# Kernel tuning notes

Hardware: AMD Instinct MI355X
Metric: run time of the kernel (lower is better)

Reference implementation:

```python
import jax, jax.numpy as jnp
import numpy as np

B, S, E, H = 4, 2048, 512, 8
D = E // H  # head dim = 64
# Faithful to torch precedence bug: embed_dim // num_heads ** 0.5 == E // (H**0.5)
SCALE = float(E // H ** 0.5)  # 181.0
EPS = 1e-5


def _ln(x, g, b):
    mu = jnp.mean(x, axis=-1, keepdims=True)
    var = jnp.var(x, axis=-1, keepdims=True)
    return (x - mu) / jnp.sqrt(var + EPS) * g + b


def setup_inputs() -> dict:
    key = jax.random.key(0)
    ks = jax.random.split(key, 14)
    inv = 1.0 / np.sqrt(E)
    inp = {
        'q': jax.random.normal(ks[0], (B, S, E), jnp.float32),
        'k': jax.random.normal(ks[1], (B, S, E), jnp.float32),
        'v': jax.random.normal(ks[2], (B, S, E), jnp.float32),
        'Wq': jax.random.uniform(ks[3], (E, E), jnp.float32, -inv, inv),
        'bq': jnp.zeros((E,), jnp.float32),
        'Wk': jax.random.uniform(ks[4], (E, E), jnp.float32, -inv, inv),
        'bk': jnp.zeros((E,), jnp.float32),
        'Wv': jax.random.uniform(ks[5], (E, E), jnp.float32, -inv, inv),
        'bv': jnp.zeros((E,), jnp.float32),
        'Wo': jax.random.uniform(ks[6], (E, E), jnp.float32, -inv, inv),
        'bo': jnp.zeros((E,), jnp.float32),
        'gq': jnp.ones((D,), jnp.float32), 'betaq': jnp.zeros((D,), jnp.float32),
        'gk': jnp.ones((D,), jnp.float32), 'betak': jnp.zeros((D,), jnp.float32),
        'gv': jnp.ones((D,), jnp.float32), 'betav': jnp.zeros((D,), jnp.float32),
        'query_mask': jax.random.uniform(ks[7], (B, S, 1)) < 0.9,
        'key_mask': jax.random.uniform(ks[8], (B, S, 1)) < 0.9,
        'value_mask': jax.random.uniform(ks[9], (B, S, 1)) < 0.9,
    }
    return inp


def reference(q, k, v, Wq, bq, Wk, bk, Wv, bv, Wo, bo,
              gq, betaq, gk, betak, gv, betav,
              query_mask, key_mask, value_mask):
    # project + mask (bool mask multiplies as 0/1)
    qp = (q @ Wq.T + bq) * query_mask            # [B,S,E]
    kp = (k @ Wk.T + bk) * key_mask
    vp = (v @ Wv.T + bv) * value_mask
    # split heads -> [B,H,S,D]
    split = lambda x: x.reshape(B, -1, H, D).transpose(0, 2, 1, 3)
    qh, kh, vh = split(qp), split(kp), split(vp)
    # middle_norm: per-head LayerNorm over head dim
    qh, kh, vh = _ln(qh, gq, betaq), _ln(kh, gk, betak), _ln(vh, gv, betav)
    scores = jnp.einsum('bhqd,bhkd->bhqk', qh, kh) / SCALE  # [B,H,S,S]
    km = key_mask[:, :, 0][:, None, None, :]     # [B,1,1,S]
    scores = jnp.where(km, scores, -1e9)
    attn = jax.nn.softmax(scores, axis=-1)
    qm = query_mask[:, :, 0][:, None, :, None]   # [B,1,S,1]
    attn = attn * qm                              # zero-fill post-softmax
    out = jnp.einsum('bhqk,bhkd->bhqd', attn, vh)
    out = out.transpose(0, 2, 1, 3).reshape(B, -1, E)
    out = (out @ Wo.T + bo) * query_mask
    return out
```

## Files before the change

### kernel.cpp

```cpp
#include <hip/hip_runtime.h>
#include <cstdint>
#include <cstddef>

#define BB 4
#define SS 2048
#define EE 512
#define HH 8
#define DD 64
#define MM (BB*SS)
#define BHSD ((size_t)BB*HH*SS*DD)

static constexpr float SCALE_INV = 1.0f / 181.0f;
static constexpr float LN_EPS = 1e-5f;

typedef float  v4f  __attribute__((ext_vector_type(4)));
typedef __bf16 v8bf __attribute__((ext_vector_type(8)));
typedef __bf16 v4bf __attribute__((ext_vector_type(4)));
typedef short  s4   __attribute__((ext_vector_type(4)));

static __device__ __forceinline__ v4f mfma16(v8bf a, v8bf b, v4f c) {
  return __builtin_amdgcn_mfma_f32_16x16x32_bf16(a, b, c, 0, 0, 0);
}
static __device__ __forceinline__ v4f mfma16x16(v4bf a, v4bf b, v4f c) {
  s4 ai = __builtin_bit_cast(s4, a);
  s4 bi = __builtin_bit_cast(s4, b);
  return __builtin_amdgcn_mfma_f32_16x16x16bf16_1k(ai, bi, c, 0, 0, 0);
}

typedef const void __attribute__((address_space(1))) gas_void;
typedef void __attribute__((address_space(3))) las_void;
static __device__ __forceinline__ void gload_lds16(const void* g, void* l) {
  __builtin_amdgcn_global_load_lds((gas_void*)g, (las_void*)l, 16, 0, 0);
}

static constexpr size_t oXb = 0;
static constexpr size_t oWb = oXb + (size_t)3*MM*EE*2;
static constexpr size_t oXh = oWb + (size_t)4*EE*EE*2;
static constexpr size_t oAO = oXh + (size_t)3*MM*EE*2;
static constexpr size_t oMk = oAO + (size_t)MM*EE*2;

__global__ void mask_kernel(const void* qm, const void* km, const void* vm, float* maskF) {
  __shared__ int s_n01, s_nF;
  const int t = threadIdx.x;
  if (t == 0) { s_n01 = 0; s_nF = 0; }
  __syncthreads();
  int n01 = 0, nF = 0;
  const unsigned* wq = (const unsigned*)qm;
  for (int i = t; i < 2048; i += 256) {
    const unsigned u = wq[i];
    if (u != 0u && u != 1u) n01 = 1;
    if (u != 0u && u != 0x3F800000u) nF = 1;
  }
  if (n01) atomicOr(&s_n01, 1);
  if (nF)  atomicOr(&s_nF, 1);
  __syncthreads();
  const int mode = (!s_n01) ? 0 : (!s_nF) ? 1 : 2;
  const int gidx = blockIdx.x * 256 + t;
  const int m = gidx / MM, i = gidx % MM;
  const void* p = (m == 0) ? qm : (m == 1) ? km : vm;
  int v;
  if (mode == 0)      v = (((const int*)p)[i] != 0);
  else if (mode == 1) v = (((const unsigned*)p)[i] != 0u);
  else                v = (((const unsigned char*)p)[i] != 0);
  maskF[m*MM + i] = v ? 1.0f : 0.0f;
}

__global__ void convert_kernel(const float* q, const float* k, const float* v,
                               const float* Wq, const float* Wk, const float* Wv, const float* Wo,
                               __bf16* Xb, __bf16* Wb) {
  const long idx = (long)blockIdx.x * 256 + threadIdx.x;
  const long NX4 = (long)3*MM*EE/4;
  const long NW4 = (long)4*EE*EE/4;
  if (idx < NX4) {
    const long per = (long)MM*EE/4;
    const long mat = idx / per, off = idx % per;
    const float* src = (mat == 0) ? q : (mat == 1) ? k : v;
    v4f val = ((const v4f*)src)[off];
    v4bf o; o[0]=(__bf16)val[0]; o[1]=(__bf16)val[1]; o[2]=(__bf16)val[2]; o[3]=(__bf16)val[3];
    ((v4bf*)Xb)[idx] = o;
  } else if (idx < NX4 + NW4) {
    const long j = idx - NX4;
    const long per = (long)EE*EE/4;
    const long mat = j / per, off = j % per;
    const float* src = (mat == 0) ? Wq : (mat == 1) ? Wk : (mat == 2) ? Wv : Wo;
    v4f val = ((const v4f*)src)[off];
    v4bf o; o[0]=(__bf16)val[0]; o[1]=(__bf16)val[1]; o[2]=(__bf16)val[2]; o[3]=(__bf16)val[3];
    ((v4bf*)Wb)[j] = o;
  }
}

__global__ __launch_bounds__(256) void gemm_proj_ln(const __bf16* Xb, const __bf16* Wb,
                                                    const float* bq, const float* bk, const float* bv,
                                                    const float* gq, const float* betaq,
                                                    const float* gk, const float* betak,
                                                    const float* gv, const float* betav,
                                                    const float* maskF, __bf16* Xh) {
  const int m0  = blockIdx.x * 128;
  const int n0  = blockIdx.y * 128;
  const int mat = blockIdx.z;
  const __bf16* A = Xb + (size_t)mat*MM*EE;
  const __bf16* W = Wb + (size_t)mat*EE*EE;
  const float* bias = (mat == 0) ? bq : (mat == 1) ? bk : bv;
  const float* gam  = (mat == 0) ? gq : (mat == 1) ? gk : gv;
  const float* bet  = (mat == 0) ? betaq : (mat == 1) ? betak : betav;

  __shared__ char smem[32768];

  const int t = threadIdx.x;
  const int lane = t & 63, w = t >> 6;
  const int wm = w >> 1, wn = w & 1;
  const int l15 = lane & 15, lg = lane >> 4;

  v4f acc[4][4];
  const v4f zf = {0.f, 0.f, 0.f, 0.f};
#pragma unroll
  for (int i = 0; i < 4; ++i)
#pragma unroll
    for (int j = 0; j < 4; ++j) acc[i][j] = zf;

  const int sr0 = (w*64 + lane) >> 2;
  const int sct = (w*64 + lane) & 3;
#define STAGE_PL(BUF, KT)                                                                 \
  {                                                                                       \
    char* ab_ = (BUF);                                                                    \
    char* bb_ = (BUF) + 8192;                                                             \
    _Pragma("unroll")                                                                     \
    for (int j_ = 0; j_ < 2; ++j_) {                                                      \
      const int r_ = sr0 + j_*64;                                                         \
      const int c_ = sct ^ (r_ & 3);                                                      \
      gload_lds16(A + (size_t)(m0 + r_)*EE + (KT) + c_*8, ab_ + j_*4096 + w*1024);        \
      gload_lds16(W + (size_t)(n0 + r_)*EE + (KT) + c_*8, bb_ + j_*4096 + w*1024);        \
    }                                                                                     \
  }

  char* buf0 = smem;
  char* buf1 = smem + 16384;

  STAGE_PL(buf0, 0);
  __syncthreads();

  int cur = 0;
  for (int kt = 0; kt < EE; kt += 32) {
    char* cb = cur ? buf1 : buf0;
    char* nb = cur ? buf0 : buf1;
    if (kt + 32 < EE) STAGE_PL(nb, kt + 32);

    const char* As = cb;
    const char* Bs = cb + 8192;
    v8bf afr[4], bfr[4];
#pragma unroll
    for (int i = 0; i < 4; ++i) {
      const int ra = wm*64 + i*16 + l15;
      afr[i] = *(const v8bf*)(As + ra*64 + ((16*lg) ^ ((ra & 3) << 4)));
      const int rb = wn*64 + i*16 + l15;
      bfr[i] = *(const v8bf*)(Bs + rb*64 + ((16*lg) ^ ((rb & 3) << 4)));
    }
#pragma unroll
    for (int i = 0; i < 4; ++i)
#pragma unroll
      for (int j = 0; j < 4; ++j)
        acc[i][j] = mfma16(afr[i], bfr[j], acc[i][j]);
    __syncthreads();
    cur ^= 1;
  }
#undef STAGE_PL

  const int nbase = n0 + wn*64;
  const int h = nbase >> 6;
  float bsv[4], gmv[4], btv[4];
#pragma unroll
  for (int j = 0; j < 4; ++j) {
    const int d = j*16 + l15;
    bsv[j] = bias[nbase + d];
    gmv[j] = gam[d];
    btv[j] = bet[d];
  }
#pragma unroll
  for (int i = 0; i < 4; ++i)
#pragma unroll
    for (int rr = 0; rr < 4; ++rr) {
      const int row = m0 + wm*64 + i*16 + 4*lg + rr;
      const float mv = maskF[mat*MM + row];
      float x[4];
      float s = 0.f, s2 = 0.f;
#pragma unroll
      for (int j = 0; j < 4; ++j) {
        x[j] = (acc[i][j][rr] + bsv[j]) * mv;
        s += x[j]; s2 += x[j]*x[j];
      }
      s  += __shfl_xor(s, 1, 64);  s  += __shfl_xor(s, 2, 64);
      s  += __shfl_xor(s, 4, 64);  s  += __shfl_xor(s, 8, 64);
      s2 += __shfl_xor(s2, 1, 64); s2 += __shfl_xor(s2, 2, 64);
      s2 += __shfl_xor(s2, 4, 64); s2 += __shfl_xor(s2, 8, 64);
      const float mu  = s * (1.0f/64.0f);
      const float var = s2 * (1.0f/64.0f) - mu*mu;
      const float rstd = rsqrtf(var + LN_EPS);
      const int bidx = row >> 11, sI = row & 2047;
      if (mat == 2) {
        const size_t vbase = 2*BHSD + (((size_t)bidx*HH + h)*DD)*SS;
#pragma unroll
        for (int j = 0; j < 4; ++j)
          Xh[vbase + (size_t)(j*16 + l15)*SS + sI] = (__bf16)((x[j] - mu)*rstd*gmv[j] + btv[j]);
      } else {
        const size_t base = (size_t)mat*BHSD + (((size_t)bidx*HH + h)*SS + sI)*DD;
#pragma unroll
        for (int j = 0; j < 4; ++j)
          Xh[base + j*16 + l15] = (__bf16)((x[j] - mu)*rstd*gmv[j] + btv[j]);
      }
    }
}

__global__ __launch_bounds__(512, 4) void attn_kernel(const __bf16* Xh, const float* maskF, __bf16* AO) {
  const int qb = blockIdx.x, h = blockIdx.y, b = blockIdx.z;
  const int t = threadIdx.x;
  const int w = t >> 6, lane = t & 63;
  const int hh = w >> 2, wq = w & 3;
  const int l15 = lane & 15, lg = lane >> 4;

  __shared__ char smem[65536];

  const size_t headoff = (((size_t)b*HH + h)*SS)*DD;
  const __bf16* Qg = Xh + headoff;
  const __bf16* Kg = Xh + BHSD + headoff;
  const __bf16* Vt = Xh + 2*BHSD + (((size_t)b*HH + h)*DD)*SS;
  const float* qmF = maskF + (size_t)b*SS;
  const float* kmF = maskF + MM + (size_t)b*SS;

  const int q0 = qb*128 + wq*32;

  v8bf qf[2][2];
#pragma unroll
  for (int m = 0; m < 2; ++m)
#pragma unroll
    for (int kd = 0; kd < 2; ++kd) {
      v8bf r = *(const v8bf*)(Qg + (size_t)(q0 + m*16 + l15)*DD + kd*32 + lg*8);
      v8bf o;
#pragma unroll
      for (int e = 0; e < 8; ++e) o[e] = (__bf16)((float)r[e] * SCALE_INV);
      qf[m][kd] = o;
    }

  v4f O[2][4];
  float lsum[2] = {0.f, 0.f};
  const v4f zf = {0.f,0.f,0.f,0.f};
#pragma unroll
  for (int m = 0; m < 2; ++m)
#pragma unroll
    for (int df = 0; df < 4; ++df) O[m][df] = zf;

  const int srow = lane >> 3;
  const int sc   = lane & 7;
#define STAGE(BUFC, KT0)                                                                \
  {                                                                                     \
    char* kb_ = (BUFC);                                                                 \
    char* vb_ = (BUFC) + 8192;                                                          \
    _Pragma("unroll")                                                                   \
    for (int j_ = 0; j_ < 2; ++j_) {                                                    \
      const int r0_ = wq*16 + j_*8;                                                     \
      const int r_  = r0_ + srow;                                                       \
      gload_lds16(Kg + (size_t)((KT0) + r_)*DD + ((sc ^ (r_ & 7))*8), kb_ + r0_*128);   \
      gload_lds16(Vt + (size_t)r_*SS + (KT0) + ((sc ^ (r_ & 7))*8),  vb_ + r0_*128);    \
    }                                                                                   \
  }

  char* bufA = smem + hh*32768;
  char* bufB = bufA + 16384;

  STAGE(bufA, (0*2 + hh)*64);
  __syncthreads();

  for (int tt = 0; tt < 16; ++tt) {
    char* cur = (tt & 1) ? bufB : bufA;
    char* nxt = (tt & 1) ? bufA : bufB;
    if (tt + 1 < 16) STAGE(nxt, ((tt+1)*2 + hh)*64);

    const int kt0 = (tt*2 + hh)*64;
    char* kb = cur;
    char* vb = cur + 8192;

    v8bf kf[4][2];
#pragma unroll
    for (int f = 0; f < 4; ++f)
#pragma unroll
      for (int kd = 0; kd < 2; ++kd) {
        const int rr = f*16 + l15;
        kf[f][kd] = *(const v8bf*)(kb + rr*128 + (((kd*4 + lg) ^ (rr & 7))*16));
      }

    v4f st[2][4];
#pragma unroll
    for (int m = 0; m < 2; ++m)
#pragma unroll
      for (int f = 0; f < 4; ++f) st[m][f] = zf;
#pragma unroll
    for (int kd = 0; kd < 2; ++kd)
#pragma unroll
      for (int f = 0; f < 4; ++f)
#pragma unroll
        for (int m = 0; m < 2; ++m)
          st[m][f] = mfma16(kf[f][kd], qf[m][kd], st[m][f]);

    v4f km4[4];
#pragma unroll
    for (int f = 0; f < 4; ++f)
      km4[f] = *(const v4f*)(kmF + kt0 + f*16 + 4*lg);

#pragma unroll
    for (int m = 0; m < 2; ++m) {
#pragma unroll
      for (int f = 0; f < 4; ++f) {
        float p[4];
#pragma unroll
        for (int rr = 0; rr < 4; ++rr) {
          p[rr] = __expf(st[m][f][rr]) * km4[f][rr];
          lsum[m] += p[rr];
        }
        v4bf pa;
        pa[0] = (__bf16)p[0]; pa[1] = (__bf16)p[1];
        pa[2] = (__bf16)p[2]; pa[3] = (__bf16)p[3];
#pragma unroll
        for (int df = 0; df < 4; ++df) {
          const int rv = df*16 + l15;
          v4bf vv = *(const v4bf*)(vb + rv*128 + (((2*f + (lg >> 1)) ^ (rv & 7))*16) + (lg & 1)*8);
          O[m][df] = mfma16x16(pa, vv, O[m][df]);
        }
      }
    }
    __syncthreads();
  }
#undef STAGE

#pragma unroll
  for (int m = 0; m < 2; ++m) {
    lsum[m] += __shfl_xor(lsum[m], 16, 64);
    lsum[m] += __shfl_xor(lsum[m], 32, 64);
  }

  float (*Pp)[32][65] = (float (*)[32][65])smem;
  float (*Lp)[32]     = (float (*)[32])(smem + 4*32*65*4);
  if (hh == 1) {
#pragma unroll
    for (int m = 0; m < 2; ++m)
#pragma unroll
      for (int df = 0; df < 4; ++df)
#pragma unroll
        for (int rr = 0; rr < 4; ++rr)
          Pp[wq][m*16 + 4*lg + rr][df*16 + l15] = O[m][df][rr];
    if (lg == 0) { Lp[wq][l15] = lsum[0]; Lp[wq][16 + l15] = lsum[1]; }
  }
  __syncthreads();
  if (hh == 0) {
#pragma unroll
    for (int m = 0; m < 2; ++m) {
      lsum[m] += Lp[wq][m*16 + l15];
#pragma unroll
      for (int df = 0; df < 4; ++df)
#pragma unroll
        for (int rr = 0; rr < 4; ++rr)
          O[m][df][rr] += Pp[wq][m*16 + 4*lg + rr][df*16 + l15];
    }
#pragma unroll
    for (int m = 0; m < 2; ++m)
#pragma unroll
      for (int rr = 0; rr < 4; ++rr) {
        const float lr = __shfl(lsum[m], (lg << 4) | (4*lg + rr), 64);
        const int qrow = q0 + m*16 + 4*lg + rr;
        const float scl = qmF[qrow] / fmaxf(lr, 1e-30f);
#pragma unroll
        for (int df = 0; df < 4; ++df)
          AO[(size_t)(b*SS + qrow)*EE + h*DD + df*16 + l15] = (__bf16)(O[m][df][rr] * scl);
      }
  }
}

__global__ __launch_bounds__(256) void gemm_out(const __bf16* AO, const __bf16* Wb,
                                                const float* bo, const float* maskF, float* out) {
  const int m0 = blockIdx.x * 128;
  const int n0 = blockIdx.y * 128;
  const __bf16* A = AO;
  const __bf16* W = Wb + (size_t)3*EE*EE;

  __shared__ char smem[32768];

  const int t = threadIdx.x;
  const int lane = t & 63, w = t >> 6;
  const int wm = w >> 1, wn = w & 1;
  const int l15 = lane & 15, lg = lane >> 4;

  v4f acc[4][4];
  const v4f zf = {0.f,0.f,0.f,0.f};
#pragma unroll
  for (int i = 0; i < 4; ++i)
#pragma unroll
    for (int j = 0; j < 4; ++j) acc[i][j] = zf;

  const int sr0 = (w*64 + lane) >> 2;
  const int sct = (w*64 + lane) & 3;
#define STAGE_PL(BUF, KT)                                                                 \
  {                                                                                       \
    char* ab_ = (BUF);                                                                    \
    char* bb_ = (BUF) + 8192;                                                             \
    _Pragma("unroll")                                                                     \
    for (int j_ = 0; j_ < 2; ++j_) {                                                      \
      const int r_ = sr0 + j_*64;                                                         \
      const int c_ = sct ^ (r_ & 3);                                                      \
      gload_lds16(A + (size_t)(m0 + r_)*EE + (KT) + c_*8, ab_ + j_*4096 + w*1024);        \
      gload_lds16(W + (size_t)(n0 + r_)*EE + (KT) + c_*8, bb_ + j_*4096 + w*1024);        \
    }                                                                                     \
  }

  char* buf0 = smem;
  char* buf1 = smem + 16384;

  STAGE_PL(buf0, 0);
  __syncthreads();

  int cur = 0;
  for (int kt = 0; kt < EE; kt += 32) {
    char* cb = cur ? buf1 : buf0;
    char* nb = cur ? buf0 : buf1;
    if (kt + 32 < EE) STAGE_PL(nb, kt + 32);

    const char* As = cb;
    const char* Bs = cb + 8192;
    v8bf afr[4], bfr[4];
#pragma unroll
    for (int i = 0; i < 4; ++i) {
      const int ra = wm*64 + i*16 + l15;
      afr[i] = *(const v8bf*)(As + ra*64 + ((16*lg) ^ ((ra & 3) << 4)));
      const int rb = wn*64 + i*16 + l15;
      bfr[i] = *(const v8bf*)(Bs + rb*64 + ((16*lg) ^ ((rb & 3) << 4)));
    }
#pragma unroll
    for (int i = 0; i < 4; ++i)
#pragma unroll
      for (int j = 0; j < 4; ++j)
        acc[i][j] = mfma16(afr[i], bfr[j], acc[i][j]);
    __syncthreads();
    cur ^= 1;
  }
#undef STAGE_PL

  float bsv[4]; int ncol[4];
#pragma unroll
  for (int j = 0; j < 4; ++j) {
    ncol[j] = n0 + wn*64 + j*16 + l15;
    bsv[j] = bo[ncol[j]];
  }
#pragma unroll
  for (int i = 0; i < 4; ++i)
#pragma unroll
    for (int rr = 0; rr < 4; ++rr) {
      const int row = m0 + wm*64 + i*16 + 4*lg + rr;
      const float mv = maskF[row];
#pragma unroll
      for (int j = 0; j < 4; ++j)
        out[(size_t)row*EE + ncol[j]] = (acc[i][j][rr] + bsv[j]) * mv;
    }
}

extern "C" void kernel_launch(void* const* d_in, const int* in_sizes, int n_in,
                              void* d_out, int out_size, void* d_ws, size_t ws_size,
                              hipStream_t stream) {
  const float* q  = (const float*)d_in[0];
  const float* k  = (const float*)d_in[1];
  const float* v  = (const float*)d_in[2];
  const float* Wq = (const float*)d_in[3];
  const float* bq = (const float*)d_in[4];
  const float* Wk = (const float*)d_in[5];
  const float* bk = (const float*)d_in[6];
  const float* Wv = (const float*)d_in[7];
  const float* bv = (const float*)d_in[8];
  const float* Wo = (const float*)d_in[9];
  const float* bo = (const float*)d_in[10];
  const float* gq = (const float*)d_in[11];
  const float* betaq = (const float*)d_in[12];
  const float* gk = (const float*)d_in[13];
  const float* betak = (const float*)d_in[14];
  const float* gv = (const float*)d_in[15];
  const float* betav = (const float*)d_in[16];

  char* ws = (char*)d_ws;
  __bf16* Xb = (__bf16*)(ws + oXb);
  __bf16* Wb = (__bf16*)(ws + oWb);
  __bf16* Xh = (__bf16*)(ws + oXh);
  __bf16* AO = (__bf16*)(ws + oAO);
  float*  maskF = (float*)(ws + oMk);

  mask_kernel<<<dim3(96), dim3(256), 0, stream>>>(d_in[17], d_in[18], d_in[19], maskF);
  convert_kernel<<<dim3(13312), dim3(256), 0, stream>>>(q, k, v, Wq, Wk, Wv, Wo, Xb, Wb);
  gemm_proj_ln<<<dim3(64, 4, 3), dim3(256), 0, stream>>>(Xb, Wb, bq, bk, bv,
                                                         gq, betaq, gk, betak, gv, betav,
                                                         maskF, Xh);
  attn_kernel<<<dim3(16, 8, 4), dim3(512), 0, stream>>>(Xh, maskF, AO);
  gemm_out<<<dim3(64, 4, 1), dim3(256), 0, stream>>>(AO, Wb, bo, maskF, (float*)d_out);
}
```

Baseline: 127.6 us.

## Use 16x16x32 MFMA for PV via permuted K rows, single-buffer LDS

Loads K rows in a permuted order (SIGMA) so that the score accumulator layout matches the A-operand layout of the 16x16x32 bf16 MFMA. The PV product can then use the wider instruction with 8-element P and V fragments instead of the 16x16x16 variant, and the key-mask indexing is permuted to match. It also drops the LDS double buffering in favour of a single buffer with a sync after each load, halving shared memory and removing the occupancy hint from launch bounds. This raises possible occupancy and halves the PV MFMA count, but gives up the overlap between global-to-LDS copies and compute.

```diff
diff --git a/kernel.cpp b/kernel.cpp
--- a/kernel.cpp
+++ b/kernel.cpp
@@ -20,11 +20,6 @@
 
 static __device__ __forceinline__ v4f mfma16(v8bf a, v8bf b, v4f c) {
   return __builtin_amdgcn_mfma_f32_16x16x32_bf16(a, b, c, 0, 0, 0);
-}
-static __device__ __forceinline__ v4f mfma16x16(v4bf a, v4bf b, v4f c) {
-  s4 ai = __builtin_bit_cast(s4, a);
-  s4 bi = __builtin_bit_cast(s4, b);
-  return __builtin_amdgcn_mfma_f32_16x16x16bf16_1k(ai, bi, c, 0, 0, 0);
 }
 
 typedef const void __attribute__((address_space(1))) gas_void;
@@ -210,14 +205,14 @@
     }
 }
 
-__global__ __launch_bounds__(512, 4) void attn_kernel(const __bf16* Xh, const float* maskF, __bf16* AO) {
+__global__ __launch_bounds__(512) void attn_kernel(const __bf16* Xh, const float* maskF, __bf16* AO) {
   const int qb = blockIdx.x, h = blockIdx.y, b = blockIdx.z;
   const int t = threadIdx.x;
   const int w = t >> 6, lane = t & 63;
   const int hh = w >> 2, wq = w & 3;
   const int l15 = lane & 15, lg = lane >> 4;
 
-  __shared__ char smem[65536];
+  __shared__ char smem[33792];
 
   const size_t headoff = (((size_t)b*HH + h)*SS)*DD;
   const __bf16* Qg = Xh + headoff;
@@ -250,33 +245,30 @@
 
   const int srow = lane >> 3;
   const int sc   = lane & 7;
-#define STAGE(BUFC, KT0)                                                                \
-  {                                                                                     \
-    char* kb_ = (BUFC);                                                                 \
-    char* vb_ = (BUFC) + 8192;                                                          \
-    _Pragma("unroll")                                                                   \
-    for (int j_ = 0; j_ < 2; ++j_) {                                                    \
-      const int r0_ = wq*16 + j_*8;                                                     \
-      const int r_  = r0_ + srow;                                                       \
-      gload_lds16(Kg + (size_t)((KT0) + r_)*DD + ((sc ^ (r_ & 7))*8), kb_ + r0_*128);   \
-      gload_lds16(Vt + (size_t)r_*SS + (KT0) + ((sc ^ (r_ & 7))*8),  vb_ + r0_*128);    \
-    }                                                                                   \
-  }
-
-  char* bufA = smem + hh*32768;
-  char* bufB = bufA + 16384;
-
-  STAGE(bufA, (0*2 + hh)*64);
-  __syncthreads();
+#define SIGMA(r) (((r) & ~31) | ((((r)>>2)&3)<<3) | ((((r)>>4)&1)<<2) | ((r)&3))
+#define STAGE1(BUFC, KT0)                                                                  \
+  {                                                                                        \
+    char* kb_ = (BUFC);                                                                    \
+    char* vb_ = (BUFC) + 8192;                                                             \
+    _Pragma("unroll")                                                                      \
+    for (int j_ = 0; j_ < 2; ++j_) {                                                       \
+      const int r0_ = wq*16 + j_*8;                                                        \
+      const int r_  = r0_ + srow;                                                          \
+      const int sg_ = SIGMA(r_);                                                           \
+      gload_lds16(Kg + (size_t)((KT0) + sg_)*DD + ((sc ^ (r_ & 7))*8), kb_ + r0_*128);     \
+      gload_lds16(Vt + (size_t)r_*SS + (KT0) + ((sc ^ (r_ & 7))*8),  vb_ + r0_*128);       \
+    }                                                                                      \
+  }
+
+  char* buf = smem + hh*16384;
 
   for (int tt = 0; tt < 16; ++tt) {
-    char* cur = (tt & 1) ? bufB : bufA;
-    char* nxt = (tt & 1) ? bufA : bufB;
-    if (tt + 1 < 16) STAGE(nxt, ((tt+1)*2 + hh)*64);
-
     const int kt0 = (tt*2 + hh)*64;
-    char* kb = cur;
-    char* vb = cur + 8192;
+    STAGE1(buf, kt0);
+    __syncthreads();
+
+    char* kb = buf;
+    char* vb = buf + 8192;
 
     v8bf kf[4][2];
 #pragma unroll
@@ -303,32 +295,37 @@
     v4f km4[4];
 #pragma unroll
     for (int f = 0; f < 4; ++f)
-      km4[f] = *(const v4f*)(kmF + kt0 + f*16 + 4*lg);
+      km4[f] = *(const v4f*)(kmF + kt0 + (f >> 1)*32 + (f & 1)*4 + 8*lg);
 
 #pragma unroll
     for (int m = 0; m < 2; ++m) {
-#pragma unroll
-      for (int f = 0; f < 4; ++f) {
-        float p[4];
+      float p[4][4];
+#pragma unroll
+      for (int f = 0; f < 4; ++f)
 #pragma unroll
         for (int rr = 0; rr < 4; ++rr) {
-          p[rr] = __expf(st[m][f][rr]) * km4[f][rr];
-          lsum[m] += p[rr];
+          p[f][rr] = __expf(st[m][f][rr]) * km4[f][rr];
+          lsum[m] += p[f][rr];
         }
-        v4bf pa;
-        pa[0] = (__bf16)p[0]; pa[1] = (__bf16)p[1];
-        pa[2] = (__bf16)p[2]; pa[3] = (__bf16)p[3];
+#pragma unroll
+      for (int g = 0; g < 2; ++g) {
+        v8bf pa;
+        pa[0] = (__bf16)p[2*g][0];   pa[1] = (__bf16)p[2*g][1];
+        pa[2] = (__bf16)p[2*g][2];   pa[3] = (__bf16)p[2*g][3];
+        pa[4] = (__bf16)p[2*g+1][0]; pa[5] = (__bf16)p[2*g+1][1];
+        pa[6] = (__bf16)p[2*g+1][2]; pa[7] = (__bf16)p[2*g+1][3];
 #pragma unroll
         for (int df = 0; df < 4; ++df) {
           const int rv = df*16 + l15;
-          v4bf vv = *(const v4bf*)(vb + rv*128 + (((2*f + (lg >> 1)) ^ (rv & 7))*16) + (lg & 1)*8);
-          O[m][df] = mfma16x16(pa, vv, O[m][df]);
+          v8bf vv = *(const v8bf*)(vb + rv*128 + (((g*4 + lg) ^ (rv & 7))*16));
+          O[m][df] = mfma16(pa, vv, O[m][df]);
         }
       }
     }
     __syncthreads();
   }
-#undef STAGE
+#undef STAGE1
+#undef SIGMA
 
 #pragma unroll
   for (int m = 0; m < 2; ++m) {
```

Measured after the change: 127.4 us. About the same (-0.2%).
